# Kernel optimization log

Hardware: AMD Instinct MI355X
Metric: run time of the kernel (lower is better)

Reference implementation:

```python
import jax, jax.numpy as jnp
import numpy as np

H = 64  # GRU hidden size


def _gru_scan(x_proj, m, U, b_rec):
    # x_proj: [S,B,3H] precomputed input projections (time-major); m: [S,B] bool mask
    B = x_proj.shape[1]
    h0 = jnp.zeros((B, H), x_proj.dtype)

    def step(h, inp):
        xp, mt = inp
        rec = h @ U + b_rec                       # [B,3H] (Keras reset_after=True)
        xz, xr, xh = jnp.split(xp, 3, axis=-1)
        rz, rr, rh = jnp.split(rec, 3, axis=-1)
        z = jax.nn.sigmoid(xz + rz)
        r = jax.nn.sigmoid(xr + rr)
        hh = jnp.tanh(xh + r * rh)
        hn = z * h + (1.0 - z) * hh
        hn = jnp.where(mt[:, None], hn, h)        # masked steps carry state through
        return hn, hn

    hT, hs = jax.lax.scan(step, h0, (x_proj, m))
    return hs, hT  # hs: [S,B,H], hT: [B,H]


def setup_inputs() -> dict:
    key = jax.random.key(0)
    ks = jax.random.split(key, 16)
    V, E = 50000, 25
    B, S, T = 512, 200, 10
    s = 0.05
    f32 = jnp.float32
    inp = {
        "input_batch": jax.random.randint(ks[0], (B, S, T), 0, V),
        "emb_table": jax.random.normal(ks[1], (V, E), f32) * s,
        "W_f": jax.random.normal(ks[2], (E, 3 * H), f32) * s,
        "U_f": jax.random.normal(ks[3], (H, 3 * H), f32) * s,
        "b_f": jnp.zeros((2, 3 * H), f32),
        "W_b": jax.random.normal(ks[4], (E, 3 * H), f32) * s,
        "U_b": jax.random.normal(ks[5], (H, 3 * H), f32) * s,
        "b_b": jnp.zeros((2, 3 * H), f32),
        "W_k": jax.random.normal(ks[6], (2 * H, H), f32) * s,
        "b_k": jnp.zeros((H,), f32),
        "W_q": jax.random.normal(ks[7], (H, H), f32) * s,
        "b_q": jnp.zeros((H,), f32),
        "W_e": jax.random.normal(ks[8], (H, 1), f32) * s,
        "b_e": jnp.zeros((1,), f32),
    }
    return inp


def reference(input_batch, emb_table, W_f, U_f, b_f, W_b, U_b, b_b, W_k, b_k, W_q, b_q, W_e, b_e):
    mask = input_batch != 0                                  # [B,S,T]
    emb = emb_table[input_batch]                             # [B,S,T,E]
    nm = mask.astype(emb.dtype)
    denom = nm.sum(axis=2)                                   # [B,S]
    denom = jnp.where(denom == 0, jnp.ones_like(denom), denom)
    x = (emb * nm[..., None]).sum(axis=2) / denom[..., None] # [B,S,E] masked mean over tags
    step_mask = mask[:, :, 0]                                # [B,S] GRU step mask

    xT = jnp.swapaxes(x, 0, 1)                               # [S,B,E]
    mT = jnp.swapaxes(step_mask, 0, 1)                       # [S,B]

    # forward GRU
    hs_f, hT_f = _gru_scan(xT @ W_f + b_f[0], mT, U_f, b_f[1])
    # backward GRU: reverse time, scan, reverse back
    hs_b, _ = _gru_scan((xT @ W_b + b_b[0])[::-1], mT[::-1], U_b, b_b[1])
    hs_b = hs_b[::-1]

    out = jnp.swapaxes(jnp.concatenate([hs_f, hs_b], axis=-1), 0, 1)  # [B,S,2H]

    # Bahdanau attention; query = forward final state
    keys = out @ W_k + b_k                                   # [B,S,H]
    queries = hT_f @ W_q + b_q                               # [B,H]
    e = jnp.tanh(keys + queries[:, None, :]) @ W_e + b_e     # [B,S,1]
    e = e + (1.0 - step_mask.astype(e.dtype))[..., None] * -1e9
    w = jax.nn.softmax(e, axis=1)                            # [B,S,1]
    context = (w * out).sum(axis=1)                          # [B,2H]
    return context
```

## Files before the change

kernel.cpp:

```cpp
#include <hip/hip_runtime.h>
#include <math.h>

#define BATCH 512
#define SEQ   200
#define TOK   10
#define EMB   25
#define HID   64
#define G3    192
#define ATILE 8
#define EMB_BLOCKS ((BATCH * SEQ) / 8)
#define RPK_BLOCKS 96

__device__ __forceinline__ float fast_sigmoid(float t) {
    float e = __expf(-t);
    return __builtin_amdgcn_rcpf(1.f + e);
}
__device__ __forceinline__ float fast_tanh(float t) {
    float e2 = __expf(2.f * t);
    return 1.f - 2.f * __builtin_amdgcn_rcpf(e2 + 1.f);
}

#define LDS_BARRIER() do {                                   \
    asm volatile("s_waitcnt lgkmcnt(0)" ::: "memory");       \
    __builtin_amdgcn_s_barrier();                            \
    asm volatile("" ::: "memory");                           \
} while (0)

__global__ __launch_bounds__(256) void emb_mean_kernel(
    const int* __restrict__ ids_g, const float* __restrict__ emb,
    const float* __restrict__ U_f, const float* __restrict__ U_b,
    float* __restrict__ x, float* __restrict__ mask, float* __restrict__ ut2)
{
    if (blockIdx.x >= EMB_BLOCKS) {
        const int eb = blockIdx.x - EMB_BLOCKS;
        const int slice = eb >> 3, c = eb & 7;
        const int dir = slice / 6, rem = slice % 6;
        const int g = rem >> 1, kh = rem & 1;
        const int t = threadIdx.x;
        const int jj = t >> 2, q = t & 3;
        const float* U = dir ? U_b : U_f;
        ut2[(size_t)eb * 256 + t] =
            U[(size_t)(kh * 32 + 4 * c + q) * G3 + g * HID + jj];
        return;
    }
    int grp  = blockIdx.x * 8 + (threadIdx.x >> 5);
    int lane = threadIdx.x & 31;
    const int* ids = ids_g + (size_t)grp * TOK;
    float acc = 0.f;
    int cnt = 0;
    #pragma unroll
    for (int t = 0; t < TOK; t++) {
        int id = ids[t];
        if (id != 0) {
            cnt++;
            if (lane < EMB) acc += emb[(size_t)id * EMB + lane];
        }
    }
    if (lane < EMB)
        x[(size_t)grp * EMB + lane] = cnt ? acc / (float)cnt : 0.f;
    if (lane == 0)
        mask[grp] = (ids[0] != 0) ? 1.f : 0.f;
}

__global__ __launch_bounds__(384) void xproj_kernel(
    const float* __restrict__ xg,
    const float* __restrict__ W_f, const float* __restrict__ b_f,
    const float* __restrict__ W_b, const float* __restrict__ b_b,
    float* __restrict__ xp)
{
    const int t   = threadIdx.x;
    const int dir = t / G3, cc = t - dir * G3;
    const int gr0 = blockIdx.x * 64;

    __shared__ __align__(16) float xsr[64][28];
    for (int i = t; i < 64 * 28; i += 384) {
        int r = i / 28, e = i - r * 28;
        xsr[r][e] = (e < EMB) ? xg[(size_t)(gr0 + r) * EMB + e] : 0.f;
    }

    const float* W  = dir ? W_b : W_f;
    const float* bb = dir ? b_b : b_f;
    float wreg[28];
    #pragma unroll
    for (int e = 0; e < EMB; e++) wreg[e] = W[(size_t)e * G3 + cc];
    #pragma unroll
    for (int e = EMB; e < 28; e++) wreg[e] = 0.f;
    const float bias = bb[cc];

    __syncthreads();

    float* op = xp + ((size_t)(dir * (BATCH * SEQ) + gr0)) * G3 + cc;
    #pragma unroll 4
    for (int r = 0; r < 64; r++) {
        const float4* xv4 = (const float4*)xsr[r];
        float a0 = bias, a1 = 0.f;
        #pragma unroll
        for (int c = 0; c < 7; c++) {
            const float4 xv = xv4[c];
            a0 = fmaf(xv.x, wreg[4 * c + 0], a0);
            a1 = fmaf(xv.y, wreg[4 * c + 1], a1);
            a0 = fmaf(xv.z, wreg[4 * c + 2], a0);
            a1 = fmaf(xv.w, wreg[4 * c + 3], a1);
        }
        op[(size_t)r * G3] = a0 + a1;
    }
}


#define DECL_U4(c) const float4 u##c = \
    *(const float4*)(ut2 + (size_t)slice * 2048 + (c) * 256 + (j << 2));

#define RECC(c) { const float4 hv = hv4[c];              \
    a0 = fmaf(hv.x, u##c.x, a0);                         \
    a1 = fmaf(hv.y, u##c.y, a1);                         \
    a0 = fmaf(hv.z, u##c.z, a0);                         \
    a1 = fmaf(hv.w, u##c.w, a1); }

__global__ __launch_bounds__(384, 2) void gru_kernel(
    const float* __restrict__ xp, const float* __restrict__ maskg,
    const float* __restrict__ b_f, const float* __restrict__ b_b,
    const float* __restrict__ ut2,
    float* __restrict__ outg, float* __restrict__ hT)
{
    const int bid = blockIdx.x;
    const int dir = bid >> 9;
    const int b   = bid & 511;
    const int tid = threadIdx.x;
    const int w   = tid >> 6;
    const int j   = tid & 63;
    const int g   = w >> 1;
    const int kh  = w & 1;
    const int slice = (dir * 3 + g) * 2 + kh;
    const int row   = (g < 2) ? (g * 2 + kh) : (4 + kh);
    const bool hxw  = (g == 2 && kh == 0);

    __shared__ float ms[SEQ];
    __shared__ __align__(16) float hsw[6][HID];
    __shared__ float chan[2][7][HID];

    if (tid < SEQ) ms[tid] = maskg[(size_t)b * SEQ + tid];
    hsw[w][j] = 0.f;

    DECL_U4(0) DECL_U4(1) DECL_U4(2) DECL_U4(3)
    DECL_U4(4) DECL_U4(5) DECL_U4(6) DECL_U4(7)

    const float* bias = dir ? b_b : b_f;
    const float b1 = (kh == 0) ? bias[G3 + g * HID + j] : 0.f;

    __syncthreads();

    const float* xpw = xp + ((size_t)(dir * (BATCH * SEQ) + b * SEQ)) * G3
                          + g * HID + j;
    const int sd = dir ? -1 : 1;
    int s = dir ? (SEQ - 1) : 0;
    float x0 = 0.f, x1 = 0.f;
    if (kh == 0) {
        x0 = xpw[(size_t)s * G3];
        x1 = xpw[(size_t)(s + sd) * G3];
    }

    float h = 0.f;
    float* ob = outg + (size_t)b * SEQ * (2 * HID) + dir * HID + j;
    int p = 0;

    for (int step = 0; step < SEQ; step++) {
        float* chp = &chan[p][0][0];

        const float4* hv4 = (const float4*)&hsw[w][kh * 32];
        float a0 = 0.f, a1 = 0.f;
        RECC(0) RECC(1) RECC(2) RECC(3) RECC(4) RECC(5) RECC(6) RECC(7)
        float part = a0 + a1;
        if (kh == 0) part += b1 + ((g < 2) ? x0 : 0.f);
        chp[row * HID + j] = part;
        if (hxw) chp[6 * HID + j] = x0;

        float x2 = 0.f;
        if (kh == 0) {
            int ip = s + 2 * sd;
            ip = ip < 0 ? 0 : (ip > SEQ - 1 ? SEQ - 1 : ip);
            x2 = xpw[(size_t)ip * G3];
        }

        LDS_BARRIER();

        {
            float z  = fast_sigmoid(chp[0 * HID + j] + chp[1 * HID + j]);
            float r  = fast_sigmoid(chp[2 * HID + j] + chp[3 * HID + j]);
            float rh =              chp[4 * HID + j] + chp[5 * HID + j];
            float hh = fast_tanh(chp[6 * HID + j] + r * rh);
            float hn = z * h + (1.f - z) * hh;
            hn = (ms[s] != 0.f) ? hn : h;
            h = hn;
            hsw[w][j] = hn;
            if (w == 0) ob[(size_t)s * (2 * HID)] = hn;
        }

        x0 = x1; x1 = x2;
        s += sd;
        p ^= 1;
    }
    if (w == 0 && dir == 0) hT[(size_t)b * HID + j] = h;
}


#define WK_LIST(M) \
  M(0)  M(1)  M(2)  M(3)  M(4)  M(5)  M(6)  M(7)  \
  M(8)  M(9)  M(10) M(11) M(12) M(13) M(14) M(15) \
  M(16) M(17) M(18) M(19) M(20) M(21) M(22) M(23) \
  M(24) M(25) M(26) M(27) M(28) M(29) M(30) M(31)

#define DECL_WK(t) const float wk##t = W_k[(size_t)(32 * wave + (t)) * HID + lane];

#define KF4(q, t0, t1, t2, t3) {                  \
    const float4 ov = o4[q];                      \
    acc0 = fmaf(ov.x, wk##t0, acc0);              \
    acc1 = fmaf(ov.y, wk##t1, acc1);              \
    acc0 = fmaf(ov.z, wk##t2, acc0);              \
    acc1 = fmaf(ov.w, wk##t3, acc1); }

__global__ __launch_bounds__(256) void attn_kernel(
    const float* __restrict__ outg, const float* __restrict__ maskg,
    const float* __restrict__ hT,
    const float* __restrict__ W_k, const float* __restrict__ b_k,
    const float* __restrict__ W_q, const float* __restrict__ b_q,
    const float* __restrict__ W_e, const float* __restrict__ b_e,
    float* __restrict__ ctx)
{
    const int b    = blockIdx.x;
    const int tid  = threadIdx.x;
    const int wave = tid >> 6;
    const int lane = tid & 63;

    __shared__ float qs[HID];
    __shared__ float es[SEQ];
    __shared__ __align__(16) float kp[ATILE][4][HID];
    __shared__ __align__(16) float psum[4][2 * HID];

    WK_LIST(DECL_WK)

    const float bkj = b_k[lane];
    const float wej = W_e[lane];
    const float be  = b_e[0];

    if (tid < HID) {
        float q = b_q[tid];
        const float* hrow = hT + (size_t)b * HID;
        #pragma unroll 8
        for (int i = 0; i < HID; i++) q = fmaf(hrow[i], W_q[i * HID + tid], q);
        qs[tid] = q;
    }
    __syncthreads();
    const float qj = qs[lane];

    for (int s0 = 0; s0 < SEQ; s0 += ATILE) {
        #pragma unroll 2
        for (int t = 0; t < ATILE; t++) {
            const int s = s0 + t;
            const float4* o4 = (const float4*)(outg +
                ((size_t)b * SEQ + s) * (2 * HID) + 32 * wave);
            float acc0 = 0.f, acc1 = 0.f;
            KF4(0,  0,  1,  2,  3)  KF4(1,  4,  5,  6,  7)
            KF4(2,  8,  9, 10, 11)  KF4(3, 12, 13, 14, 15)
            KF4(4, 16, 17, 18, 19)  KF4(5, 20, 21, 22, 23)
            KF4(6, 24, 25, 26, 27)  KF4(7, 28, 29, 30, 31)
            kp[t][wave][lane] = acc0 + acc1;
        }
        __syncthreads();
        #pragma unroll
        for (int t = wave; t < ATILE; t += 4) {
            const int s = s0 + t;
            float k = (kp[t][0][lane] + kp[t][1][lane]) +
                      (kp[t][2][lane] + kp[t][3][lane]);
            float v = tanhf(k + bkj + qj) * wej;
            #pragma unroll
            for (int off = 32; off > 0; off >>= 1) v += __shfl_xor(v, off);
            if (lane == 0) {
                float pen = (maskg[(size_t)b * SEQ + s] != 0.f) ? 0.f : -1e9f;
                es[s] = v + be + pen;
            }
        }
        __syncthreads();
    }

    if (tid < 64) {
        float mx = -1e30f;
        for (int s2 = tid; s2 < SEQ; s2 += 64) mx = fmaxf(mx, es[s2]);
        #pragma unroll
        for (int off = 32; off > 0; off >>= 1) mx = fmaxf(mx, __shfl_xor(mx, off));
        float sum = 0.f;
        for (int s2 = tid; s2 < SEQ; s2 += 64) {
            float w = expf(es[s2] - mx);
            es[s2] = w;
            sum += w;
        }
        #pragma unroll
        for (int off = 32; off > 0; off >>= 1) sum += __shfl_xor(sum, off);
        float inv = 1.f / sum;
        for (int s2 = tid; s2 < SEQ; s2 += 64) es[s2] *= inv;
    }
    __syncthreads();

    {
        float a0 = 0.f, a1 = 0.f;
        #pragma unroll 2
        for (int s2 = wave; s2 < SEQ; s2 += 4) {
            const float2 v = *(const float2*)(outg +
                ((size_t)b * SEQ + s2) * (2 * HID) + lane * 2);
            const float wsc = es[s2];
            a0 = fmaf(wsc, v.x, a0);
            a1 = fmaf(wsc, v.y, a1);
        }
        psum[wave][2 * lane]     = a0;
        psum[wave][2 * lane + 1] = a1;
    }
    __syncthreads();
    if (tid < 2 * HID) {
        ctx[(size_t)b * (2 * HID) + tid] =
            (psum[0][tid] + psum[1][tid]) + (psum[2][tid] + psum[3][tid]);
    }
}

extern "C" void kernel_launch(void* const* d_in, const int* in_sizes, int n_in,
                              void* d_out, int out_size, void* d_ws, size_t ws_size,
                              hipStream_t stream) {
    const int*   ids = (const int*)  d_in[0];
    const float* emb = (const float*)d_in[1];
    const float* W_f = (const float*)d_in[2];
    const float* U_f = (const float*)d_in[3];
    const float* b_f = (const float*)d_in[4];
    const float* W_b = (const float*)d_in[5];
    const float* U_b = (const float*)d_in[6];
    const float* b_b = (const float*)d_in[7];
    const float* W_k = (const float*)d_in[8];
    const float* b_k = (const float*)d_in[9];
    const float* W_q = (const float*)d_in[10];
    const float* b_q = (const float*)d_in[11];
    const float* W_e = (const float*)d_in[12];
    const float* b_e = (const float*)d_in[13];

    float* ws   = (float*)d_ws;
    float* x    = ws;
    float* mask = ws + 2560000;
    float* out  = ws + 2662400;
    float* hT   = ws + 15769600;
    float* ut2  = ws + 15802368;
    float* xp   = ws + 15826944;

    emb_mean_kernel<<<EMB_BLOCKS + RPK_BLOCKS, 256, 0, stream>>>(
        ids, emb, U_f, U_b, x, mask, ut2);
    xproj_kernel<<<(BATCH * SEQ) / 64, 384, 0, stream>>>(
        x, W_f, b_f, W_b, b_b, xp);
    gru_kernel<<<1024, 384, 0, stream>>>(xp, mask, b_f, b_b, ut2, out, hT);
    attn_kernel<<<BATCH, 256, 0, stream>>>(out, mask, hT, W_k, b_k,
                                           W_q, b_q, W_e, b_e, (float*)d_out);
}
```

Baseline: 501.5 us.

## Reload GRU recurrent weights per step from a transposed layout instead of registers

The recurrent weight slice is repacked so each thread owns 32 contiguous floats, and the GRU loop reloads it from global memory (L1/L2) every timestep instead of keeping 32 values resident in registers. An asm barrier on the pointer stops the compiler from hoisting the loads back out. The aim is to free VGPRs and cut register pressure. The gate channel buffer in LDS is padded to a row stride of 72, and the xp and output addressing becomes pointer increments. The prefetch clamp is dropped, so the last steps read past the sequence into neighbouring data that is never used. The trade is eight extra vector loads per thread on the serial critical path of every step, and those loads have strided lane access.

```diff
diff --git a/kernel.cpp b/kernel.cpp
--- a/kernel.cpp
+++ b/kernel.cpp
@@ -29,18 +29,18 @@
 __global__ __launch_bounds__(256) void emb_mean_kernel(
     const int* __restrict__ ids_g, const float* __restrict__ emb,
     const float* __restrict__ U_f, const float* __restrict__ U_b,
-    float* __restrict__ x, float* __restrict__ mask, float* __restrict__ ut2)
+    float* __restrict__ x, float* __restrict__ mask, float* __restrict__ ut3)
 {
     if (blockIdx.x >= EMB_BLOCKS) {
         const int eb = blockIdx.x - EMB_BLOCKS;
-        const int slice = eb >> 3, c = eb & 7;
+        const int slice = eb >> 3, sub = eb & 7;
         const int dir = slice / 6, rem = slice % 6;
         const int g = rem >> 1, kh = rem & 1;
-        const int t = threadIdx.x;
-        const int jj = t >> 2, q = t & 3;
+        const int idx = sub * 256 + threadIdx.x;
+        const int jj = idx >> 5, k = idx & 31;
         const float* U = dir ? U_b : U_f;
-        ut2[(size_t)eb * 256 + t] =
-            U[(size_t)(kh * 32 + 4 * c + q) * G3 + g * HID + jj];
+        ut3[(size_t)slice * 2048 + idx] =
+            U[(size_t)(kh * 32 + k) * G3 + g * HID + jj];
         return;
     }
     int grp  = blockIdx.x * 8 + (threadIdx.x >> 5);
@@ -107,9 +107,6 @@
 }
 
 
-#define DECL_U4(c) const float4 u##c = \
-    *(const float4*)(ut2 + (size_t)slice * 2048 + (c) * 256 + (j << 2));
-
 #define RECC(c) { const float4 hv = hv4[c];              \
     a0 = fmaf(hv.x, u##c.x, a0);                         \
     a1 = fmaf(hv.y, u##c.y, a1);                         \
@@ -119,7 +116,7 @@
 __global__ __launch_bounds__(384, 2) void gru_kernel(
     const float* __restrict__ xp, const float* __restrict__ maskg,
     const float* __restrict__ b_f, const float* __restrict__ b_b,
-    const float* __restrict__ ut2,
+    const float* __restrict__ ut3,
     float* __restrict__ outg, float* __restrict__ hT)
 {
     const int bid = blockIdx.x;
@@ -136,66 +133,77 @@
 
     __shared__ float ms[SEQ];
     __shared__ __align__(16) float hsw[6][HID];
-    __shared__ float chan[2][7][HID];
+    __shared__ float chan[2][7][72];
 
     if (tid < SEQ) ms[tid] = maskg[(size_t)b * SEQ + tid];
     hsw[w][j] = 0.f;
 
-    DECL_U4(0) DECL_U4(1) DECL_U4(2) DECL_U4(3)
-    DECL_U4(4) DECL_U4(5) DECL_U4(6) DECL_U4(7)
-
     const float* bias = dir ? b_b : b_f;
     const float b1 = (kh == 0) ? bias[G3 + g * HID + j] : 0.f;
 
     __syncthreads();
 
-    const float* xpw = xp + ((size_t)(dir * (BATCH * SEQ) + b * SEQ)) * G3
+    const float* ubase = ut3 + (size_t)slice * 2048 + (j << 5);
+
+    const int sd = dir ? -1 : 1;
+    const int pstride = sd * G3;
+    int s = dir ? (SEQ - 1) : 0;
+    const float* xpp = xp + ((size_t)(dir * (BATCH * SEQ) + b * SEQ + s)) * G3
                           + g * HID + j;
-    const int sd = dir ? -1 : 1;
-    int s = dir ? (SEQ - 1) : 0;
     float x0 = 0.f, x1 = 0.f;
     if (kh == 0) {
-        x0 = xpw[(size_t)s * G3];
-        x1 = xpw[(size_t)(s + sd) * G3];
+        x0 = xpp[0];
+        x1 = xpp[pstride];
     }
 
     float h = 0.f;
-    float* ob = outg + (size_t)b * SEQ * (2 * HID) + dir * HID + j;
+    float* ob = outg + (size_t)b * SEQ * (2 * HID) + (size_t)s * (2 * HID)
+                     + dir * HID + j;
+    const int obstride = sd * (2 * HID);
     int p = 0;
 
     for (int step = 0; step < SEQ; step++) {
         float* chp = &chan[p][0][0];
+
+        const float* up = ubase;
+        asm volatile("" : "+v"(up));
+        const float4 u0 = *(const float4*)(up + 0);
+        const float4 u1 = *(const float4*)(up + 4);
+        const float4 u2 = *(const float4*)(up + 8);
+        const float4 u3 = *(const float4*)(up + 12);
+        const float4 u4 = *(const float4*)(up + 16);
+        const float4 u5 = *(const float4*)(up + 20);
+        const float4 u6 = *(const float4*)(up + 24);
+        const float4 u7 = *(const float4*)(up + 28);
 
         const float4* hv4 = (const float4*)&hsw[w][kh * 32];
         float a0 = 0.f, a1 = 0.f;
         RECC(0) RECC(1) RECC(2) RECC(3) RECC(4) RECC(5) RECC(6) RECC(7)
         float part = a0 + a1;
         if (kh == 0) part += b1 + ((g < 2) ? x0 : 0.f);
-        chp[row * HID + j] = part;
-        if (hxw) chp[6 * HID + j] = x0;
+        chp[row * 72 + j] = part;
+        if (hxw) chp[6 * 72 + j] = x0;
 
         float x2 = 0.f;
-        if (kh == 0) {
-            int ip = s + 2 * sd;
-            ip = ip < 0 ? 0 : (ip > SEQ - 1 ? SEQ - 1 : ip);
-            x2 = xpw[(size_t)ip * G3];
-        }
+        if (kh == 0) x2 = xpp[2 * pstride];
 
         LDS_BARRIER();
 
         {
-            float z  = fast_sigmoid(chp[0 * HID + j] + chp[1 * HID + j]);
-            float r  = fast_sigmoid(chp[2 * HID + j] + chp[3 * HID + j]);
-            float rh =              chp[4 * HID + j] + chp[5 * HID + j];
-            float hh = fast_tanh(chp[6 * HID + j] + r * rh);
+            float z  = fast_sigmoid(chp[0 * 72 + j] + chp[1 * 72 + j]);
+            float r  = fast_sigmoid(chp[2 * 72 + j] + chp[3 * 72 + j]);
+            float rh =              chp[4 * 72 + j] + chp[5 * 72 + j];
+            float hh = fast_tanh(chp[6 * 72 + j] + r * rh);
             float hn = z * h + (1.f - z) * hh;
             hn = (ms[s] != 0.f) ? hn : h;
             h = hn;
             hsw[w][j] = hn;
-            if (w == 0) ob[(size_t)s * (2 * HID)] = hn;
+            if (w == 0) *ob = hn;
         }
 
         x0 = x1; x1 = x2;
+        xpp += pstride;
+        ob  += obstride;
         s += sd;
         p ^= 1;
     }
@@ -343,14 +351,14 @@
     float* mask = ws + 2560000;
     float* out  = ws + 2662400;
     float* hT   = ws + 15769600;
-    float* ut2  = ws + 15802368;
+    float* ut3  = ws + 15802368;
     float* xp   = ws + 15826944;
 
     emb_mean_kernel<<<EMB_BLOCKS + RPK_BLOCKS, 256, 0, stream>>>(
-        ids, emb, U_f, U_b, x, mask, ut2);
+        ids, emb, U_f, U_b, x, mask, ut3);
     xproj_kernel<<<(BATCH * SEQ) / 64, 384, 0, stream>>>(
         x, W_f, b_f, W_b, b_b, xp);
-    gru_kernel<<<1024, 384, 0, stream>>>(xp, mask, b_f, b_b, ut2, out, hT);
+    gru_kernel<<<1024, 384, 0, stream>>>(xp, mask, b_f, b_b, ut3, out, hT);
     attn_kernel<<<BATCH, 256, 0, stream>>>(out, mask, hT, W_k, b_k,
                                            W_q, b_q, W_e, b_e, (float*)d_out);
 }
```

Result: slower. 1.396 ms (+178.3%).
